# Kernel tuning notes

Measured on AMD Instinct MI355X. Metric: run time of the kernel, lower is better.

## Reference

```python
import jax, jax.numpy as jnp
import numpy as np

DIM = 768
N_IMGS = 1024
N_PATCH = 196
GRID = int(np.sqrt(N_PATCH))  # 14
B = 64


def setup_inputs() -> dict:
    key = jax.random.key(0)
    ks = jax.random.split(key, 12)
    x = jax.random.normal(ks[0], (B, N_PATCH, DIM), dtype=jnp.float32)
    mask = jnp.ones((B, N_PATCH), dtype=jnp.bool_)
    img_ids = jax.random.randint(ks[1], (B,), 0, N_IMGS, dtype=jnp.int32)
    eps = jax.random.normal(ks[2], (B, 2, N_PATCH), dtype=jnp.float32)
    s = 0.02
    Wq = jax.random.normal(ks[3], (DIM, DIM), dtype=jnp.float32) * s
    bq = jnp.zeros((DIM,), dtype=jnp.float32)
    Wk = jax.random.normal(ks[4], (DIM, DIM), dtype=jnp.float32) * s
    bk = jnp.zeros((DIM,), dtype=jnp.float32)
    Wv = jax.random.normal(ks[5], (DIM, DIM), dtype=jnp.float32) * s
    bv = jnp.zeros((DIM,), dtype=jnp.float32)
    # per-image Gaussian location params: means in [0, GRID-1], small positive stds
    avgs = jax.random.uniform(ks[6], (N_IMGS, 2, N_PATCH), dtype=jnp.float32) * (GRID - 1)
    std_devs = jax.random.uniform(ks[7], (N_IMGS, 2, N_PATCH), dtype=jnp.float32) * 1.5 + 0.1
    return {"x": x, "mask": mask, "img_ids": img_ids, "eps": eps,
            "Wq": Wq, "bq": bq, "Wk": Wk, "bk": bk, "Wv": Wv, "bv": bv,
            "avgs": avgs, "std_devs": std_devs}


def reference(x, mask, img_ids, eps, Wq, bq, Wk, bk, Wv, bv, avgs, std_devs):
    # projections: (B,S,D)
    q = jnp.einsum('bsd,ed->bse', x, Wq) + bq
    k = jnp.einsum('bsd,ed->bse', x, Wk) + bk
    v = jnp.einsum('bsd,ed->bse', x, Wv) + bv

    # sample per-query key coordinates: torch.normal(mean, std) == mean + std * eps
    mu = avgs[img_ids]        # (B,2,S)
    sd = std_devs[img_ids]    # (B,2,S)
    coord = mu + sd * eps     # (B,2,S)
    kx, ky = coord[:, 0], coord[:, 1]           # each (B,S)
    kx1, kx2 = jnp.ceil(kx), jnp.floor(kx)
    ky1, ky2 = jnp.ceil(ky), jnp.floor(ky)

    # 4 interpolation-corner flat indices per query: grid*y + x  -> (B,S,4)
    idx = jnp.stack([GRID * ky1 + kx1,
                     GRID * ky1 + kx2,
                     GRID * ky2 + kx1,
                     GRID * ky2 + kx2], axis=-1)
    idx = jnp.clip(idx, 0, N_PATCH - 1).astype(jnp.int32)

    bidx = jnp.arange(idx.shape[0])[:, None, None]  # (B,1,1)
    sampled_k = k[bidx, idx]  # (B,S,4,D)
    sampled_v = v[bidx, idx]  # (B,S,4,D)

    # softmax over the 4 sampled keys (elementwise per feature), weighted sum of values
    w = jax.nn.softmax(q[:, :, None, :] * sampled_k, axis=2)  # (B,S,4,D)
    out = jnp.sum(w * sampled_v, axis=2)                      # (B,S,D)
    return out
```

## Files before the change

kernel.cpp:

```cpp
#include <hip/hip_runtime.h>
#include <hip/hip_bf16.h>

typedef _Float16 f16;
typedef f16 f16x4 __attribute__((ext_vector_type(4)));
typedef f16 f16x8 __attribute__((ext_vector_type(8)));
typedef float f32x4 __attribute__((ext_vector_type(4)));

#define DIM   768
#define NP    196
#define BATCH 64
#define MROWS (BATCH * NP)
#define NCOLS (3 * DIM)
#define GRIDF 14.0f

#define NX4   (MROWS * DIM / 4)
#define NW4   (DIM * DIM / 4)
#define NB4   (NCOLS / 4)
#define NCVTA (NX4 + 3 * NW4 + NB4)

__global__ __launch_bounds__(256) void convert_inputs(
    const float* __restrict__ x,
    const float* __restrict__ Wq, const float* __restrict__ Wk, const float* __restrict__ Wv,
    const float* __restrict__ bq, const float* __restrict__ bk, const float* __restrict__ bv,
    f16* __restrict__ x_h, f16* __restrict__ W_h, float* __restrict__ bias_all) {
  int i = blockIdx.x * 256 + threadIdx.x;
  if (i >= NCVTA) return;
  if (i < NX4 + 3 * NW4) {
    const float* src;
    f16* dst;
    int j;
    if (i < NX4) { src = x; dst = x_h; j = i; }
    else {
      j = i - NX4;
      if (j < NW4)          { src = Wq; dst = W_h; }
      else if (j < 2 * NW4) { src = Wk; dst = W_h + DIM * DIM;     j -= NW4; }
      else                  { src = Wv; dst = W_h + 2 * DIM * DIM; j -= 2 * NW4; }
    }
    float4 v = ((const float4*)src)[j];
    f16x4 h;
    h[0] = (f16)v.x; h[1] = (f16)v.y; h[2] = (f16)v.z; h[3] = (f16)v.w;
    ((f16x4*)dst)[j] = h;
  } else {
    int j = i - (NX4 + 3 * NW4);
    float4 v = (j < 192) ? ((const float4*)bq)[j]
             : (j < 384) ? ((const float4*)bk)[j - 192]
                         : ((const float4*)bv)[j - 384];
    ((float4*)bias_all)[j] = v;
  }
}


#define BM 256
#define BN 256
#define BK 64
#define NT    (DIM / BK)
#define NITER (NT / 2)

__device__ __forceinline__ void gl_lds16(const f16* g, f16* l) {
  __builtin_amdgcn_global_load_lds(
      (const __attribute__((address_space(1))) void*)g,
      (__attribute__((address_space(3))) void*)l, 16, 0, 0);
}

#define MFMA16(acc_, av, bv) acc_ = __builtin_amdgcn_mfma_f32_16x16x32_f16(av, bv, acc_, 0, 0, 0)
#define BAR    __builtin_amdgcn_s_barrier()
#define LGKM0  asm volatile("s_waitcnt lgkmcnt(0)" ::: "memory")
#define VMCNT4 asm volatile("s_waitcnt vmcnt(4)" ::: "memory")
#define VMCNT0 asm volatile("s_waitcnt vmcnt(0)" ::: "memory")

#define sAoff(buf) ((buf) * (BM * BK))
#define sBoff(buf) (2 * BM * BK + (buf) * (BN * BK))

__global__ __launch_bounds__(512, 2) void gemm_qkv(
    const f16* __restrict__ A, const f16* __restrict__ W,
    const float* __restrict__ bias_all, f16* __restrict__ C) {
  __shared__ __align__(16) f16 lds[2 * BM * BK + 2 * BN * BK];

  const int t    = threadIdx.x;
  const int lane = t & 63;
  const int wid  = t >> 6;
  const int wr   = wid >> 2;
  const int wc   = wid & 3;

  const int nwg = 49 * 9, qq = nwg / 8, rr = nwg % 8;
  const int xcd = blockIdx.x & 7, seq = blockIdx.x >> 3;
  const int logical = (xcd < rr ? xcd * (qq + 1) : rr * (qq + 1) + (xcd - rr) * qq) + seq;
  const int bm0 = (logical / 9) * BM;
  const int bn0 = (logical % 9) * BN;

  const int srow  = t >> 3;
  const int sslot = t & 7;
  const int gcol  = 8 * (sslot ^ (srow & 7));
  const int lds_off = srow * BK + sslot * 8;
  const f16* gAr = A + (size_t)(bm0 + srow) * DIM + gcol;
  const f16* gBr = W + (size_t)(bn0 + srow) * DIM + gcol;

#define STAGE_A(kt, h) do {                                          \
    const f16* _g = gAr + (size_t)((h) * 128) * DIM + (kt) * BK;     \
    f16* _l = &lds[sAoff((kt) & 1) + (h) * 128 * BK + lds_off];      \
    gl_lds16(_g, _l);                                                \
    gl_lds16(_g + (size_t)64 * DIM, _l + 64 * BK);                   \
  } while (0)

#define STAGE_B(kt, h) do {                                          \
    const f16* _g = gBr + (size_t)((h) * 128) * DIM + (kt) * BK;     \
    f16* _l = &lds[sBoff((kt) & 1) + (h) * 128 * BK + lds_off];      \
    gl_lds16(_g, _l);                                                \
    gl_lds16(_g + (size_t)64 * DIM, _l + 64 * BK);                   \
  } while (0)

  const int rl = lane & 15;
  const int kg = lane >> 4;
  const int s7 = lane & 7;
  const int slot0 = ((0 * 4 + kg) ^ s7) * 8;
  const int slot1 = ((1 * 4 + kg) ^ s7) * 8;
  const int aBase = (wr * 128 + rl) * BK;
  const int bBase = (wc * 64 + rl) * BK;

  f32x4 acc[8][4] = {};
  f16x8 afr[2][2], bfr[4][2];

#define LDB(buf) do {                                                                   \
    _Pragma("unroll") for (int ni = 0; ni < 4; ++ni) {                                  \
      bfr[ni][0] = *(const f16x8*)&lds[sBoff(buf) + bBase + ni * 16 * BK + slot0];      \
      bfr[ni][1] = *(const f16x8*)&lds[sBoff(buf) + bBase + ni * 16 * BK + slot1];      \
    } } while (0)

#define LDA(buf, q_) do {                                                               \
    _Pragma("unroll") for (int mm = 0; mm < 2; ++mm) {                                  \
      afr[mm][0] = *(const f16x8*)&lds[sAoff(buf) + aBase + ((q_) * 2 + mm) * 16 * BK + slot0]; \
      afr[mm][1] = *(const f16x8*)&lds[sAoff(buf) + aBase + ((q_) * 2 + mm) * 16 * BK + slot1]; \
    } } while (0)

#define MMA(q_) do {                                                                    \
    __builtin_amdgcn_s_setprio(1);                                                      \
    _Pragma("unroll") for (int ni = 0; ni < 4; ++ni) {                                  \
      MFMA16(acc[(q_) * 2 + 0][ni], bfr[ni][0], afr[0][0]);                             \
      MFMA16(acc[(q_) * 2 + 1][ni], bfr[ni][0], afr[1][0]);                             \
      MFMA16(acc[(q_) * 2 + 0][ni], bfr[ni][1], afr[0][1]);                             \
      MFMA16(acc[(q_) * 2 + 1][ni], bfr[ni][1], afr[1][1]);                             \
    }                                                                                   \
    __builtin_amdgcn_s_setprio(0); } while (0)

  STAGE_A(0, 0); STAGE_A(0, 1); STAGE_B(0, 0); STAGE_B(0, 1);
  STAGE_B(1, 0); STAGE_B(1, 1);
  VMCNT4;
  BAR;

  for (int i = 0; i < NITER; ++i) {
    const int t1 = 2 * i + 1;
    const bool more = (i + 1 < NITER);
    LDB(0); LDA(0, 0); STAGE_A(t1, 0);
    BAR; LGKM0; MMA(0); BAR;
    LDA(0, 1); STAGE_A(t1, 1);
    BAR; LGKM0; MMA(1); BAR;
    LDA(0, 2); if (more) STAGE_B(t1 + 1, 0);
    BAR; LGKM0; MMA(2); BAR;
    LDA(0, 3); if (more) STAGE_B(t1 + 1, 1);
    BAR; LGKM0; MMA(3);
    if (more) { VMCNT4; } else { VMCNT0; }
    BAR;
    LDB(1); LDA(1, 0); if (more) STAGE_A(t1 + 1, 0);
    BAR; LGKM0; MMA(0); BAR;
    LDA(1, 1); if (more) STAGE_A(t1 + 1, 1);
    BAR; LGKM0; MMA(1); BAR;
    LDA(1, 2); if (more) STAGE_B(t1 + 2, 0);
    BAR; LGKM0; MMA(2); BAR;
    LDA(1, 3); if (more) STAGE_B(t1 + 2, 1);
    BAR; LGKM0; MMA(3); VMCNT4; BAR;
  }

  {
    const int mloc0 = wr * 128 + rl;
    const int nq0   = wc * 64 + 4 * kg;
#pragma unroll
    for (int ni = 0; ni < 4; ++ni) {
      const int nloc = nq0 + ni * 16;
      const float4 b4 = *(const float4*)&bias_all[bn0 + nloc];
#pragma unroll
      for (int mi = 0; mi < 8; ++mi) {
        const int m = mloc0 + mi * 16;
        f16x4 h;
        h[0] = (f16)(acc[mi][ni][0] + b4.x);
        h[1] = (f16)(acc[mi][ni][1] + b4.y);
        h[2] = (f16)(acc[mi][ni][2] + b4.z);
        h[3] = (f16)(acc[mi][ni][3] + b4.w);
        *(f16x4*)&lds[m * 256 + (nloc ^ ((m & 7) << 3))] = h;
      }
    }
    LGKM0; BAR;
    const int rrow = t >> 5;
    const int rchk = t & 31;
#pragma unroll
    for (int p = 0; p < 16; ++p) {
      const int row = p * 16 + rrow;
      f16x8 vdat = *(const f16x8*)&lds[row * 256 + ((rchk * 8) ^ ((row & 7) << 3))];
      *(f16x8*)&C[(size_t)(bm0 + row) * NCOLS + bn0 + rchk * 8] = vdat;
    }
  }
}

__global__ __launch_bounds__(256) void attend(
    const f16* __restrict__ qkv,
    const int* __restrict__ img_ids, const float* __restrict__ eps,
    const float* __restrict__ avgs, const float* __restrict__ stds,
    float* __restrict__ out) {
  const int lane = threadIdx.x & 63;
  const int wid  = threadIdx.x >> 6;
  const int logical = (blockIdx.x & 7) * 392 + (blockIdx.x >> 3);
  const int gw = logical * 4 + wid;
  const int b = gw / NP;
  const int s = gw - b * NP;

  const int img = img_ids[b];
  const float ex = eps[(b * 2 + 0) * NP + s];
  const float ey = eps[(b * 2 + 1) * NP + s];
  const float mux = avgs[(img * 2 + 0) * NP + s];
  const float muy = avgs[(img * 2 + 1) * NP + s];
  const float sdx = stds[(img * 2 + 0) * NP + s];
  const float sdy = stds[(img * 2 + 1) * NP + s];

  const float kx = fmaf(sdx, ex, mux);
  const float ky = fmaf(sdy, ey, muy);
  const float kx1 = ceilf(kx), kx2 = floorf(kx);
  const float ky1 = ceilf(ky), ky2 = floorf(ky);

  int idx[4];
  idx[0] = (int)fminf(fmaxf(GRIDF * ky1 + kx1, 0.0f), 195.0f);
  idx[1] = (int)fminf(fmaxf(GRIDF * ky1 + kx2, 0.0f), 195.0f);
  idx[2] = (int)fminf(fmaxf(GRIDF * ky2 + kx1, 0.0f), 195.0f);
  idx[3] = (int)fminf(fmaxf(GRIDF * ky2 + kx2, 0.0f), 195.0f);

  const f16* qrow = qkv + (size_t)gw * NCOLS;
  const f16* base = qkv + (size_t)(b * NP) * NCOLS;
  const f16* k0p = base + (size_t)idx[0] * NCOLS + DIM;
  const f16* k1p = base + (size_t)idx[1] * NCOLS + DIM;
  const f16* k2p = base + (size_t)idx[2] * NCOLS + DIM;
  const f16* k3p = base + (size_t)idx[3] * NCOLS + DIM;
  const f16* v0p = k0p + DIM;
  const f16* v1p = k1p + DIM;
  const f16* v2p = k2p + DIM;
  const f16* v3p = k3p + DIM;
  float* orow = out + (size_t)gw * DIM;

#pragma unroll
  for (int seg = 0; seg < 3; ++seg) {
    const int e0 = seg * 256 + lane * 4;
    f16x4 qv  = *(const f16x4*)(qrow + e0);
    f16x4 kv0 = *(const f16x4*)(k0p + e0);
    f16x4 kv1 = *(const f16x4*)(k1p + e0);
    f16x4 kv2 = *(const f16x4*)(k2p + e0);
    f16x4 kv3 = *(const f16x4*)(k3p + e0);
    f16x4 vv0 = *(const f16x4*)(v0p + e0);
    f16x4 vv1 = *(const f16x4*)(v1p + e0);
    f16x4 vv2 = *(const f16x4*)(v2p + e0);
    f16x4 vv3 = *(const f16x4*)(v3p + e0);
    float4 o;
    float* op = &o.x;
#pragma unroll
    for (int c = 0; c < 4; ++c) {
      const float q = (float)qv[c];
      const float s0 = q * (float)kv0[c];
      const float s1 = q * (float)kv1[c];
      const float s2 = q * (float)kv2[c];
      const float s3 = q * (float)kv3[c];
      const float mx = fmaxf(fmaxf(s0, s1), fmaxf(s2, s3));
      const float w0 = __expf(s0 - mx);
      const float w1 = __expf(s1 - mx);
      const float w2 = __expf(s2 - mx);
      const float w3 = __expf(s3 - mx);
      const float den = w0 + w1 + w2 + w3;
      const float num = w0 * (float)vv0[c] + w1 * (float)vv1[c] +
                        w2 * (float)vv2[c] + w3 * (float)vv3[c];
      op[c] = num / den;
    }
    *(float4*)(orow + e0) = o;
  }
}

extern "C" void kernel_launch(void* const* d_in, const int* in_sizes, int n_in,
                              void* d_out, int out_size, void* d_ws, size_t ws_size,
                              hipStream_t stream) {
  const float* x       = (const float*)d_in[0];
  const int*   img_ids = (const int*)d_in[2];
  const float* eps     = (const float*)d_in[3];
  const float* Wq      = (const float*)d_in[4];
  const float* bq      = (const float*)d_in[5];
  const float* Wk      = (const float*)d_in[6];
  const float* bk      = (const float*)d_in[7];
  const float* Wv      = (const float*)d_in[8];
  const float* bv      = (const float*)d_in[9];
  const float* avgs    = (const float*)d_in[10];
  const float* stds    = (const float*)d_in[11];
  float* out = (float*)d_out;

  char* ws = (char*)d_ws;
  const size_t XH_BYTES = (size_t)MROWS * DIM * 2;
  const size_t WH_BYTES = (size_t)NCOLS * DIM * 2;
  const size_t BI_BYTES = (size_t)NCOLS * 4;
  f16*   x_h      = (f16*)ws;
  f16*   W_h      = (f16*)(ws + XH_BYTES);
  float* bias_all = (float*)(ws + XH_BYTES + WH_BYTES);
  f16*   qkv      = (f16*)(ws + XH_BYTES + WH_BYTES + BI_BYTES);

  {
    int grid = (NCVTA + 255) / 256;
    convert_inputs<<<grid, 256, 0, stream>>>(x, Wq, Wk, Wv, bq, bk, bv, x_h, W_h, bias_all);
  }
  {
    gemm_qkv<<<441, 512, 0, stream>>>(x_h, W_h, bias_all, qkv);
  }
  {
    int grid = MROWS / 4;
    attend<<<grid, 256, 0, stream>>>(qkv, img_ids, eps, avgs, stds, out);
  }
}
```

Measured before the change: 83.82 us.

## Shrink QKV GEMM tiles to 128x128x32 with 256-thread blocks

Replaces the 256x256x64 tile GEMM using 512 threads with a 128x128x32 tile using 256 threads and four blocks per CU, rewriting the swizzle, LDS staging, MFMA schedule and epilogue to match. The intent is more blocks and better occupancy/latency hiding across CUs. The trade-off is lower data reuse per tile, more LDS and global traffic per flop, more barriers per K step, and a partial final wave.

```diff
diff --git a/kernel.cpp b/kernel.cpp
--- a/kernel.cpp
+++ b/kernel.cpp
@@ -50,11 +50,10 @@
 }
 
 
-#define BM 256
-#define BN 256
-#define BK 64
-#define NT    (DIM / BK)
-#define NITER (NT / 2)
+#define BM 128
+#define BN 128
+#define BK 32
+#define NT (DIM / BK)
 
 __device__ __forceinline__ void gl_lds16(const f16* g, f16* l) {
   __builtin_amdgcn_global_load_lds(
@@ -71,130 +70,116 @@
 #define sAoff(buf) ((buf) * (BM * BK))
 #define sBoff(buf) (2 * BM * BK + (buf) * (BN * BK))
 
-__global__ __launch_bounds__(512, 2) void gemm_qkv(
+__global__ __launch_bounds__(256, 4) void gemm_qkv(
     const f16* __restrict__ A, const f16* __restrict__ W,
     const float* __restrict__ bias_all, f16* __restrict__ C) {
-  __shared__ __align__(16) f16 lds[2 * BM * BK + 2 * BN * BK];
+  __shared__ __align__(16) f16 lds[4 * BM * BK];
 
   const int t    = threadIdx.x;
   const int lane = t & 63;
   const int wid  = t >> 6;
-  const int wr   = wid >> 2;
-  const int wc   = wid & 3;
-
-  const int nwg = 49 * 9, qq = nwg / 8, rr = nwg % 8;
+  const int wr   = wid >> 1;
+  const int wc   = wid & 1;
+
+  const int nwg = 98 * 18, qq = nwg / 8, rr = nwg % 8;
   const int xcd = blockIdx.x & 7, seq = blockIdx.x >> 3;
   const int logical = (xcd < rr ? xcd * (qq + 1) : rr * (qq + 1) + (xcd - rr) * qq) + seq;
-  const int bm0 = (logical / 9) * BM;
-  const int bn0 = (logical % 9) * BN;
-
-  const int srow  = t >> 3;
-  const int sslot = t & 7;
-  const int gcol  = 8 * (sslot ^ (srow & 7));
+  const int bm0 = (logical / 18) * BM;
+  const int bn0 = (logical % 18) * BN;
+
+  const int srow  = t >> 2;
+  const int sslot = t & 3;
+  const int sswz  = (srow & 3) ^ ((srow >> 2) & 3);
+  const int gcol  = 8 * (sslot ^ sswz);
   const int lds_off = srow * BK + sslot * 8;
   const f16* gAr = A + (size_t)(bm0 + srow) * DIM + gcol;
   const f16* gBr = W + (size_t)(bn0 + srow) * DIM + gcol;
 
-#define STAGE_A(kt, h) do {                                          \
-    const f16* _g = gAr + (size_t)((h) * 128) * DIM + (kt) * BK;     \
-    f16* _l = &lds[sAoff((kt) & 1) + (h) * 128 * BK + lds_off];      \
+#define STAGE_A(kt) do {                                             \
+    const f16* _g = gAr + (kt) * BK;                                 \
+    f16* _l = &lds[sAoff((kt) & 1) + lds_off];                       \
     gl_lds16(_g, _l);                                                \
     gl_lds16(_g + (size_t)64 * DIM, _l + 64 * BK);                   \
   } while (0)
 
-#define STAGE_B(kt, h) do {                                          \
-    const f16* _g = gBr + (size_t)((h) * 128) * DIM + (kt) * BK;     \
-    f16* _l = &lds[sBoff((kt) & 1) + (h) * 128 * BK + lds_off];      \
+#define STAGE_B(kt) do {                                             \
+    const f16* _g = gBr + (kt) * BK;                                 \
+    f16* _l = &lds[sBoff((kt) & 1) + lds_off];                       \
     gl_lds16(_g, _l);                                                \
     gl_lds16(_g + (size_t)64 * DIM, _l + 64 * BK);                   \
   } while (0)
 
   const int rl = lane & 15;
   const int kg = lane >> 4;
-  const int s7 = lane & 7;
-  const int slot0 = ((0 * 4 + kg) ^ s7) * 8;
-  const int slot1 = ((1 * 4 + kg) ^ s7) * 8;
-  const int aBase = (wr * 128 + rl) * BK;
-  const int bBase = (wc * 64 + rl) * BK;
-
-  f32x4 acc[8][4] = {};
-  f16x8 afr[2][2], bfr[4][2];
-
-#define LDB(buf) do {                                                                   \
-    _Pragma("unroll") for (int ni = 0; ni < 4; ++ni) {                                  \
-      bfr[ni][0] = *(const f16x8*)&lds[sBoff(buf) + bBase + ni * 16 * BK + slot0];      \
-      bfr[ni][1] = *(const f16x8*)&lds[sBoff(buf) + bBase + ni * 16 * BK + slot1];      \
-    } } while (0)
-
-#define LDA(buf, q_) do {                                                               \
-    _Pragma("unroll") for (int mm = 0; mm < 2; ++mm) {                                  \
-      afr[mm][0] = *(const f16x8*)&lds[sAoff(buf) + aBase + ((q_) * 2 + mm) * 16 * BK + slot0]; \
-      afr[mm][1] = *(const f16x8*)&lds[sAoff(buf) + aBase + ((q_) * 2 + mm) * 16 * BK + slot1]; \
-    } } while (0)
-
-#define MMA(q_) do {                                                                    \
-    __builtin_amdgcn_s_setprio(1);                                                      \
-    _Pragma("unroll") for (int ni = 0; ni < 4; ++ni) {                                  \
-      MFMA16(acc[(q_) * 2 + 0][ni], bfr[ni][0], afr[0][0]);                             \
-      MFMA16(acc[(q_) * 2 + 1][ni], bfr[ni][0], afr[1][0]);                             \
-      MFMA16(acc[(q_) * 2 + 0][ni], bfr[ni][1], afr[0][1]);                             \
-      MFMA16(acc[(q_) * 2 + 1][ni], bfr[ni][1], afr[1][1]);                             \
-    }                                                                                   \
+  const int lswz = (rl & 3) ^ ((rl >> 2) & 3);
+  const int slotF = ((kg ^ lswz) & 3) * 8;
+  const int aBase = (wr * 64 + rl) * BK + slotF;
+  const int bBase = (wc * 64 + rl) * BK + slotF;
+
+  f32x4 acc[4][4] = {};
+  f16x8 afr[4], bfr[4];
+
+#define LDB(buf) do {                                                            \
+    _Pragma("unroll") for (int ni = 0; ni < 4; ++ni)                             \
+      bfr[ni] = *(const f16x8*)&lds[sBoff(buf) + bBase + ni * 16 * BK];          \
+    } while (0)
+
+#define LDA(buf) do {                                                            \
+    _Pragma("unroll") for (int mi = 0; mi < 4; ++mi)                             \
+      afr[mi] = *(const f16x8*)&lds[sAoff(buf) + aBase + mi * 16 * BK];          \
+    } while (0)
+
+#define MMA2(m0_) do {                                                           \
+    __builtin_amdgcn_s_setprio(1);                                               \
+    _Pragma("unroll") for (int ni = 0; ni < 4; ++ni) {                           \
+      MFMA16(acc[(m0_) + 0][ni], bfr[ni], afr[(m0_) + 0]);                       \
+      MFMA16(acc[(m0_) + 1][ni], bfr[ni], afr[(m0_) + 1]);                       \
+    }                                                                            \
     __builtin_amdgcn_s_setprio(0); } while (0)
 
-  STAGE_A(0, 0); STAGE_A(0, 1); STAGE_B(0, 0); STAGE_B(0, 1);
-  STAGE_B(1, 0); STAGE_B(1, 1);
+  STAGE_A(0); STAGE_B(0);
+  STAGE_A(1); STAGE_B(1);
   VMCNT4;
   BAR;
 
-  for (int i = 0; i < NITER; ++i) {
-    const int t1 = 2 * i + 1;
-    const bool more = (i + 1 < NITER);
-    LDB(0); LDA(0, 0); STAGE_A(t1, 0);
-    BAR; LGKM0; MMA(0); BAR;
-    LDA(0, 1); STAGE_A(t1, 1);
-    BAR; LGKM0; MMA(1); BAR;
-    LDA(0, 2); if (more) STAGE_B(t1 + 1, 0);
-    BAR; LGKM0; MMA(2); BAR;
-    LDA(0, 3); if (more) STAGE_B(t1 + 1, 1);
-    BAR; LGKM0; MMA(3);
+  for (int kt = 0; kt < NT; ++kt) {
+    const int b = kt & 1;
+    const bool more = (kt + 2 < NT);
+    LDB(b); LDA(b);
+    BAR; LGKM0;
+    MMA2(0);
+    BAR;
+    if (more) { STAGE_A(kt + 2); STAGE_B(kt + 2); }
+    MMA2(2);
     if (more) { VMCNT4; } else { VMCNT0; }
     BAR;
-    LDB(1); LDA(1, 0); if (more) STAGE_A(t1 + 1, 0);
-    BAR; LGKM0; MMA(0); BAR;
-    LDA(1, 1); if (more) STAGE_A(t1 + 1, 1);
-    BAR; LGKM0; MMA(1); BAR;
-    LDA(1, 2); if (more) STAGE_B(t1 + 2, 0);
-    BAR; LGKM0; MMA(2); BAR;
-    LDA(1, 3); if (more) STAGE_B(t1 + 2, 1);
-    BAR; LGKM0; MMA(3); VMCNT4; BAR;
   }
 
   {
-    const int mloc0 = wr * 128 + rl;
+    const int eRow0 = wr * 64 + rl;
     const int nq0   = wc * 64 + 4 * kg;
 #pragma unroll
     for (int ni = 0; ni < 4; ++ni) {
       const int nloc = nq0 + ni * 16;
       const float4 b4 = *(const float4*)&bias_all[bn0 + nloc];
 #pragma unroll
-      for (int mi = 0; mi < 8; ++mi) {
-        const int m = mloc0 + mi * 16;
+      for (int mi = 0; mi < 4; ++mi) {
+        const int e = eRow0 + mi * 16;
         f16x4 h;
         h[0] = (f16)(acc[mi][ni][0] + b4.x);
         h[1] = (f16)(acc[mi][ni][1] + b4.y);
         h[2] = (f16)(acc[mi][ni][2] + b4.z);
         h[3] = (f16)(acc[mi][ni][3] + b4.w);
-        *(f16x4*)&lds[m * 256 + (nloc ^ ((m & 7) << 3))] = h;
+        *(f16x4*)&lds[e * 128 + (nloc ^ ((e & 7) << 3))] = h;
       }
     }
     LGKM0; BAR;
-    const int rrow = t >> 5;
-    const int rchk = t & 31;
-#pragma unroll
-    for (int p = 0; p < 16; ++p) {
+    const int rrow = t >> 4;
+    const int rchk = t & 15;
+#pragma unroll
+    for (int p = 0; p < 8; ++p) {
       const int row = p * 16 + rrow;
-      f16x8 vdat = *(const f16x8*)&lds[row * 256 + ((rchk * 8) ^ ((row & 7) << 3))];
+      f16x8 vdat = *(const f16x8*)&lds[row * 128 + ((rchk * 8) ^ ((row & 7) << 3))];
       *(f16x8*)&C[(size_t)(bm0 + row) * NCOLS + bn0 + rchk * 8] = vdat;
     }
   }
@@ -308,7 +293,7 @@
     convert_inputs<<<grid, 256, 0, stream>>>(x, Wq, Wk, Wv, bq, bk, bv, x_h, W_h, bias_all);
   }
   {
-    gemm_qkv<<<441, 512, 0, stream>>>(x_h, W_h, bias_all, qkv);
+    gemm_qkv<<<1764, 256, 0, stream>>>(x_h, W_h, bias_all, qkv);
   }
   {
     int grid = MROWS / 4;
```

New measurement: 93.80 us. 1.12x slower.
